# Kernel optimization log

Measured on AMD Instinct MI355X. Metric: run time of the kernel, lower is better.

## Reference

```python
import jax, jax.numpy as jnp
import numpy as np

B, L, C, N, TN = 1, 256, 128, 4, 4
CH = N * C  # 512, flattened hidden for routing projections
EPS = 1.1920929e-07  # torch.finfo(float32).eps (RMSNorm default eps)
LN_EPS = 1e-5
N_SINKHORN = 20  # training-mode iteration count


def sinkhorn_knopp(raw, n_iters):
    # raw: [..., n, n] real-valued logits -> doubly-stochastic matrix
    M = jnp.exp(raw)
    for _ in range(n_iters):
        M = M / jnp.sum(M, axis=-1, keepdims=True)  # row normalize
        M = M / jnp.sum(M, axis=-2, keepdims=True)  # col normalize
    return M


def setup_inputs() -> dict:
    key = jax.random.key(0)
    ks = jax.random.split(key, 8)
    s = 0.02
    eye = jnp.eye(N, dtype=jnp.float32)
    b_res = 2.0 * eye + (-2.0) * (1.0 - eye)
    return {
        "p": jax.random.normal(ks[0], (B, L, L, C), jnp.float32),
        "p_mask": jnp.ones((B, L, L), jnp.float32),
        "W_pre": jax.random.normal(ks[1], (N, CH), jnp.float32) * s,
        "W_post": jax.random.normal(ks[2], (N, CH), jnp.float32) * s,
        "W_res": jax.random.normal(ks[3], (N * N, CH), jnp.float32) * s,
        "b_pre": jnp.zeros((1, N), jnp.float32),
        "b_post": jnp.zeros((1, N), jnp.float32),
        "b_res": b_res,
        "alpha_pre": jnp.asarray(0.01, jnp.float32),
        "alpha_post": jnp.asarray(0.01, jnp.float32),
        "alpha_res": jnp.asarray(0.01, jnp.float32),
        "ln_g": jnp.ones((C,), jnp.float32),
        "ln_b": jnp.zeros((C,), jnp.float32),
        "W1": jax.random.normal(ks[4], (TN * C, C), jnp.float32) * s,
        "b1": jnp.zeros((TN * C,), jnp.float32),
        "W2": jax.random.normal(ks[5], (C, TN * C), jnp.float32) * s,
        "b2": jnp.zeros((C,), jnp.float32),
    }


def reference(p, p_mask, W_pre, W_post, W_res, b_pre, b_post, b_res,
              alpha_pre, alpha_post, alpha_res, ln_g, ln_b, W1, b1, W2, b2):
    # expand_input: [B,L,L,C] -> [B,L,L,n,C]
    x = jnp.broadcast_to(p[..., None, :], (B, L, L, N, C))
    # --- compute_mappings ---
    xf = x.reshape(B, L, L, CH)
    xn = xf * jax.lax.rsqrt(jnp.mean(xf * xf, axis=-1, keepdims=True) + EPS)
    H_pre_dyn = jnp.tanh(xn @ W_pre.T)                      # [B,L,L,n]
    H_post_dyn = jnp.tanh(xn @ W_post.T)                    # [B,L,L,n]
    H_res_dyn = jnp.tanh(xn @ W_res.T).reshape(B, L, L, N, N)
    H_pre = jax.nn.sigmoid(alpha_pre * H_pre_dyn + b_pre)   # [B,L,L,n]
    H_post = 2.0 * jax.nn.sigmoid(alpha_post * H_post_dyn + b_post)
    H_res = sinkhorn_knopp(alpha_res * H_res_dyn + b_res, N_SINKHORN)  # [B,L,L,n,n]
    # contract: H_pre [B,L,L,1,n] @ x [B,L,L,n,C] -> [B,L,L,C]
    p_c = jnp.einsum('blkn,blknc->blkc', H_pre, x)
    # --- PairTransition (LN -> Linear -> ReLU -> Linear, masked) ---
    mu = jnp.mean(p_c, axis=-1, keepdims=True)
    var = jnp.mean(jnp.square(p_c - mu), axis=-1, keepdims=True)
    m = (p_c - mu) * jax.lax.rsqrt(var + LN_EPS) * ln_g + ln_b
    h = jax.nn.relu(m @ W1.T + b1)                          # [B,L,L,TN*C]
    p_t = (h @ W2.T + b2) * p_mask[..., None]
    p_updated = p_c + p_t
    # expand back: H_post^T [B,L,L,n,1] * p_updated [B,L,L,1,C]
    p_expanded = H_post[..., :, None] * p_updated[..., None, :]
    # residual mixing: [B,L,L,n,n] @ [B,L,L,n,C]
    p_residual = jnp.einsum('blkmn,blknc->blkmc', H_res, x)
    return p_residual + p_expanded  # [B,L,L,n,C]
```

## Files before the change

### kernel.cpp

```cpp
#include <hip/hip_runtime.h>
#include <stdint.h>

#define LLTOT 65536
#define CDIM  128
#define TPIX  32

typedef float f32x4  __attribute__((ext_vector_type(4)));
typedef short s16x8  __attribute__((ext_vector_type(8)));

#define MFMA16(a, b, c) __builtin_amdgcn_mfma_f32_16x16x32_bf16((a), (b), (c), 0, 0, 0)

__device__ __align__(16) unsigned short g_wefff[2 * 4 * 64 * 8];
__device__ __align__(16) unsigned short g_w1gf[32 * 4 * 64 * 8];
__device__ __align__(16) unsigned short g_w2f16[16 * 8 * 64 * 8];
__device__ __align__(16) float  g_hA[512];
__device__ __align__(16) float  g_w1gs[512];

__device__ __forceinline__ unsigned short f2bf(float f) {
    union { float f; uint32_t u; } v; v.f = f;
    uint32_t u = v.u;
    return (unsigned short)((u + 0x7FFFu + ((u >> 16) & 1u)) >> 16);
}
__device__ __forceinline__ uint32_t pack2(float a, float b) {
    uint32_t r;
    asm("v_cvt_pk_bf16_f32 %0, %1, %2" : "=v"(r) : "v"(a), "v"(b));
    return r;
}
__device__ __forceinline__ float bf2f(uint32_t lo16) { return __uint_as_float(lo16 << 16); }

__device__ __forceinline__ float fast_tanh(float x) {
    float cx = fminf(fmaxf(x, -10.f), 10.f);
    float e = __expf(2.f * cx);
    return (e - 1.f) * __builtin_amdgcn_rcpf(e + 1.f);
}
__device__ __forceinline__ float fast_sig(float z) {
    return __builtin_amdgcn_rcpf(1.f + __expf(-z));
}

__global__ void prep_kernel(const float* __restrict__ Wpre, const float* __restrict__ Wpost,
                            const float* __restrict__ Wres, const float* __restrict__ W1,
                            const float* __restrict__ W2, const float* __restrict__ ln_g,
                            const float* __restrict__ ln_b, const float* __restrict__ b1) {
    int b = blockIdx.x, t = threadIdx.x;
    if (b == 264) {
        int j = t;
        float sg = 0.f, sb = 0.f;
        const float* row = W1 + j * 128;
        #pragma unroll 4
        for (int c = 0; c < 128; c += 4) {
            float4 wv = *(const float4*)(row + c);
            float4 gv = *(const float4*)(ln_g + c);
            float4 bv = *(const float4*)(ln_b + c);
            sg += wv.x*gv.x + wv.y*gv.y + wv.z*gv.z + wv.w*gv.w;
            sb += wv.x*bv.x + wv.y*bv.y + wv.z*bv.z + wv.w*bv.w;
        }
        g_hA[j]   = b1[j] + sb;
        g_w1gs[j] = sg;
        return;
    }
    int idx = b * 512 + t;
    if (idx < 4096) {
        int e = idx & 7, lane = (idx >> 3) & 63, kk = (idx >> 9) & 3, tile = idx >> 11;
        int o = tile * 16 + (lane & 15);
        int c = kk * 32 + (lane >> 4) * 8 + e;
        float v = 0.f;
        if (o < 4)        v = Wpre[o*512+c] + Wpre[o*512+128+c] + Wpre[o*512+256+c] + Wpre[o*512+384+c];
        else if (o < 8)   { int j = o - 4;  v = Wpost[j*512+c] + Wpost[j*512+128+c] + Wpost[j*512+256+c] + Wpost[j*512+384+c]; }
        else if (o < 24)  { int j = o - 8;  v = Wres[j*512+c] + Wres[j*512+128+c] + Wres[j*512+256+c] + Wres[j*512+384+c]; }
        g_wefff[idx] = f2bf(v);
    } else if (idx < 69632) {
        int d = idx - 4096;
        int e = d & 7, lane = (d >> 3) & 63, kk = (d >> 9) & 3, jt = d >> 11;
        int j = jt * 16 + (lane & 15);
        int c = kk * 32 + (lane >> 4) * 8 + e;
        g_w1gf[d] = f2bf(W1[j * 128 + c] * ln_g[c]);
    } else if (idx < 135168) {
        int d = idx - 69632;
        int e = d & 7, lane = (d >> 3) & 63, ct = (d >> 9) & 7, ksg = d >> 12;
        int c = ct * 16 + (lane & 15);
        int k = ksg * 32 + (lane >> 4) * 8 + e;
        g_w2f16[d] = f2bf(W2[c * 512 + k]);
    }
}

__global__ void __launch_bounds__(512, 2) fused_kernel(
    const float* __restrict__ p, const float* __restrict__ p_mask,
    const float* __restrict__ b_pre, const float* __restrict__ b_post, const float* __restrict__ b_res,
    const float* __restrict__ a_pre, const float* __restrict__ a_post, const float* __restrict__ a_res,
    const float* __restrict__ b2g, float* __restrict__ out)
{
    __shared__ __align__(16) unsigned short pf_lds[8 * 512];
    __shared__ __align__(16) unsigned short h16[32 * 512];
    __shared__ __align__(16) float A_s[128], B_s[128];
    __shared__ __align__(16) float2 simi_s[32];
    __shared__ __align__(16) float rms_s[32], mu_s[32], var_s[32];

    const int t = threadIdx.x;
    const int w = t >> 6, l = t & 63, lr = l & 15, lk = l >> 4;
    const size_t base = (size_t)blockIdx.x * TPIX;

    s16x8 aw01[8];
    #pragma unroll
    for (int kk = 0; kk < 2; ++kk)
        #pragma unroll
        for (int jt = 0; jt < 4; ++jt)
            aw01[kk * 4 + jt] = *(const s16x8*)(g_w1gf + ((size_t)((w * 4 + jt) * 4 + kk) * 64 + l) * 8);

    {
        int pix32 = t >> 4, ci = t & 15;
        const float* src = p + (base + pix32) * 128 + ci * 8;
        float4 va = *(const float4*)src;
        float4 vb = *(const float4*)(src + 4);
        float s  = va.x + va.y + va.z + va.w + vb.x + vb.y + vb.z + vb.w;
        float ss = va.x*va.x + va.y*va.y + va.z*va.z + va.w*va.w
                 + vb.x*vb.x + vb.y*vb.y + vb.z*vb.z + vb.w*vb.w;
        s += __shfl_xor(s, 1); ss += __shfl_xor(ss, 1);
        s += __shfl_xor(s, 2); ss += __shfl_xor(ss, 2);
        s += __shfl_xor(s, 4); ss += __shfl_xor(ss, 4);
        s += __shfl_xor(s, 8); ss += __shfl_xor(ss, 8);
        if (ci == 0) {
            float mu = s * (1.f / 128.f), mq = ss * (1.f / 128.f);
            rms_s[pix32] = rsqrtf(mq + 1.1920929e-07f);
            mu_s[pix32]  = mu;
            var_s[pix32] = mq - mu * mu;
        }
        uint4 u;
        u.x = pack2(va.x, va.y);
        u.y = pack2(va.z, va.w);
        u.z = pack2(vb.x, vb.y);
        u.w = pack2(vb.z, vb.w);
        uint32_t a16 = (uint32_t)((((pix32 >> 4) * 4 + (ci >> 2)) * 512
                     + ((pix32 & 15) + 16 * (ci & 3)) * 8));
        *(uint4*)(pf_lds + a16) = u;
    }
    __syncthreads();

    float M0 = 0.f, M1 = 0.f, M2 = 0.f, M3 = 0.f, sp = 0.f, hpm = 0.f;
    int mrow = 0, pix = 0;

    if (w < 2) {
        const int g = lk, pixl = lr;
        const size_t gpix = base + w * 16 + pixl;
        float apre = a_pre[0], apost = a_post[0], ares = a_res[0];
        float msk = p_mask[gpix];
        float bp0 = b_pre[0], bp1 = b_pre[1], bp2 = b_pre[2], bp3 = b_pre[3];
        float bq0 = b_post[0], bq1 = b_post[1], bq2 = b_post[2], bq3 = b_post[3];
        mrow = (g + 2) & 3;
        float br0 = b_res[mrow*4+0], br1 = b_res[mrow*4+1], br2 = b_res[mrow*4+2], br3 = b_res[mrow*4+3];

        float rv = rms_s[w * 16 + pixl];

        f32x4 y1 = {0.f, 0.f, 0.f, 0.f}, y2 = {0.f, 0.f, 0.f, 0.f};
        #pragma unroll
        for (int kk = 0; kk < 4; ++kk) {
            s16x8 bfr = *(const s16x8*)(pf_lds + (size_t)(w * 4 + kk) * 512 + l * 8);
            s16x8 a0 = *(const s16x8*)(g_wefff + ((size_t)(kk) * 64 + l) * 8);
            s16x8 a1 = *(const s16x8*)(g_wefff + ((size_t)(4 + kk) * 64 + l) * 8);
            y1 = MFMA16(a0, bfr, y1);
            y2 = MFMA16(a1, bfr, y2);
        }
        #pragma unroll
        for (int r = 0; r < 4; ++r) { y1[r] *= rv; y2[r] *= rv; }

        float sp_loc = fast_sig(apre * fast_tanh(y1[0]) + bp0)
                     + fast_sig(apre * fast_tanh(y1[1]) + bp1)
                     + fast_sig(apre * fast_tanh(y1[2]) + bp2)
                     + fast_sig(apre * fast_tanh(y1[3]) + bp3);
        sp = __shfl(sp_loc, pixl);

        float hp0 = 2.f * fast_sig(apost * fast_tanh(y1[0]) + bq0);
        float hp1 = 2.f * fast_sig(apost * fast_tanh(y1[1]) + bq1);
        float hp2 = 2.f * fast_sig(apost * fast_tanh(y1[2]) + bq2);
        float hp3 = 2.f * fast_sig(apost * fast_tanh(y1[3]) + bq3);

        bool lo = g < 2;
        M0 = __expf(ares * fast_tanh(lo ? y2[0] : y1[0]) + br0);
        M1 = __expf(ares * fast_tanh(lo ? y2[1] : y1[1]) + br1);
        M2 = __expf(ares * fast_tanh(lo ? y2[2] : y1[2]) + br2);
        M3 = __expf(ares * fast_tanh(lo ? y2[3] : y1[3]) + br3);

        float h0b = __shfl(hp0, pixl + 16);
        float h1b = __shfl(hp1, pixl + 16);
        float h2b = __shfl(hp2, pixl + 16);
        float h3b = __shfl(hp3, pixl + 16);
        hpm = (mrow & 2) ? ((mrow & 1) ? h3b : h2b) : ((mrow & 1) ? h1b : h0b);

        pix = w * 16 + pixl;
        B_s[pix * 4 + mrow] = hpm * msk;
        if (l < 16) {
            int px = w * 16 + lr;
            float istd = rsqrtf(sp * sp * var_s[px] + 1e-5f);
            simi_s[px] = make_float2(sp * istd, sp * mu_s[px] * istd);
        }
    }
    __syncthreads();

    if (w < 2) {
        #pragma unroll 1
        for (int it = 0; it < 20; ++it) {
            float ri = __builtin_amdgcn_rcpf(M0 + M1 + M2 + M3);
            M0 *= ri; M1 *= ri; M2 *= ri; M3 *= ri;
            float c0 = M0, c1 = M1, c2 = M2, c3 = M3;
            c0 += __shfl_xor(c0, 16); c1 += __shfl_xor(c1, 16); c2 += __shfl_xor(c2, 16); c3 += __shfl_xor(c3, 16);
            c0 += __shfl_xor(c0, 32); c1 += __shfl_xor(c1, 32); c2 += __shfl_xor(c2, 32); c3 += __shfl_xor(c3, 32);
            M0 *= __builtin_amdgcn_rcpf(c0); M1 *= __builtin_amdgcn_rcpf(c1);
            M2 *= __builtin_amdgcn_rcpf(c2); M3 *= __builtin_amdgcn_rcpf(c3);
        }
        float rm = M0 + M1 + M2 + M3;
        A_s[pix * 4 + mrow] = rm + hpm * sp;
    }

    s16x8 pfr[2][4];
    #pragma unroll
    for (int it = 0; it < 2; ++it)
        #pragma unroll
        for (int kk = 0; kk < 4; ++kk)
            pfr[it][kk] = *(const s16x8*)(pf_lds + (size_t)(it * 4 + kk) * 512 + l * 8);

    f32x4 acc1[4][2] = {};
    #pragma unroll
    for (int kk = 0; kk < 2; ++kk)
        #pragma unroll
        for (int jt = 0; jt < 4; ++jt) {
            s16x8 a = aw01[kk * 4 + jt];
            acc1[jt][0] = MFMA16(a, pfr[0][kk], acc1[jt][0]);
            acc1[jt][1] = MFMA16(a, pfr[1][kk], acc1[jt][1]);
        }
    #pragma unroll
    for (int kk = 2; kk < 4; ++kk)
        #pragma unroll
        for (int jt = 0; jt < 4; ++jt) {
            s16x8 a = *(const s16x8*)(g_w1gf + ((size_t)((w * 4 + jt) * 4 + kk) * 64 + l) * 8);
            acc1[jt][0] = MFMA16(a, pfr[0][kk], acc1[jt][0]);
            acc1[jt][1] = MFMA16(a, pfr[1][kk], acc1[jt][1]);
        }

    {
        float2 sim0 = simi_s[lr];
        float2 sim1 = simi_s[16 + lr];
        #pragma unroll
        for (int jt = 0; jt < 4; ++jt) {
            int j0 = w * 64 + jt * 16 + lk * 4;
            float4 wg = *(const float4*)(g_w1gs + j0);
            float4 ha = *(const float4*)(g_hA + j0);
            int ksg = w * 2 + (jt >> 1);
            int laneB = lr + 16 * ((jt & 1) * 2 + (lk >> 1));
            #pragma unroll
            for (int it = 0; it < 2; ++it) {
                float si = it ? sim1.x : sim0.x;
                float mi = it ? sim1.y : sim0.y;
                f32x4 v = acc1[jt][it];
                float h0 = fmaxf(fmaf(si, v[0], fmaf(-mi, wg.x, ha.x)), 0.f);
                float h1 = fmaxf(fmaf(si, v[1], fmaf(-mi, wg.y, ha.y)), 0.f);
                float h2 = fmaxf(fmaf(si, v[2], fmaf(-mi, wg.z, ha.z)), 0.f);
                float h3 = fmaxf(fmaf(si, v[3], fmaf(-mi, wg.w, ha.w)), 0.f);
                uint2 uu;
                uu.x = pack2(h0, h1);
                uu.y = pack2(h2, h3);
                *(uint2*)(h16 + (size_t)(ksg * 2 + it) * 512 + laneB * 8 + (lk & 1) * 4) = uu;
            }
        }
    }
    __syncthreads();

    f32x4 acc2[2] = {};
    #pragma unroll 4
    for (int ksg = 0; ksg < 16; ++ksg) {
        s16x8 a  = *(const s16x8*)(g_w2f16 + ((size_t)(ksg * 8 + w) * 64 + l) * 8);
        s16x8 b0 = *(const s16x8*)(h16 + (size_t)(ksg * 2 + 0) * 512 + l * 8);
        s16x8 b1 = *(const s16x8*)(h16 + (size_t)(ksg * 2 + 1) * 512 + l * 8);
        acc2[0] = MFMA16(a, b0, acc2[0]);
        acc2[1] = MFMA16(a, b1, acc2[1]);
    }

    const int c0 = w * 16 + lk * 4;
    float4 b2v = *(const float4*)(b2g + c0);
    #pragma unroll
    for (int it = 0; it < 2; ++it) {
        int i = it * 16 + lr;
        f32x4 Av = *(const f32x4*)(A_s + i * 4);
        f32x4 Bv = *(const f32x4*)(B_s + i * 4);
        const unsigned short* pe = pf_lds
            + ((size_t)(it * 4 + (w >> 1)) * 64 + ((w & 1) * 2 + (lk >> 1)) * 16 + lr) * 8
            + (lk & 1) * 4;
        uint2 pb = *(const uint2*)pe;
        float p0 = bf2f(pb.x & 0xffffu), p1 = __uint_as_float(pb.x & 0xffff0000u);
        float p2 = bf2f(pb.y & 0xffffu), p3 = __uint_as_float(pb.y & 0xffff0000u);
        float d0 = acc2[it][0] + b2v.x, d1 = acc2[it][1] + b2v.y;
        float d2 = acc2[it][2] + b2v.z, d3 = acc2[it][3] + b2v.w;
        float* og = out + (base + i) * 512 + c0;
        #pragma unroll
        for (int m = 0; m < 4; ++m) {
            f32x4 o;
            o[0] = Av[m] * p0 + Bv[m] * d0;
            o[1] = Av[m] * p1 + Bv[m] * d1;
            o[2] = Av[m] * p2 + Bv[m] * d2;
            o[3] = Av[m] * p3 + Bv[m] * d3;
            *(f32x4*)(og + m * 128) = o;
        }
    }
}

extern "C" void kernel_launch(void* const* d_in, const int* in_sizes, int n_in,
                              void* d_out, int out_size, void* d_ws, size_t ws_size,
                              hipStream_t stream) {
    const float* p      = (const float*)d_in[0];
    const float* p_mask = (const float*)d_in[1];
    const float* W_pre  = (const float*)d_in[2];
    const float* W_post = (const float*)d_in[3];
    const float* W_res  = (const float*)d_in[4];
    const float* b_pre  = (const float*)d_in[5];
    const float* b_post = (const float*)d_in[6];
    const float* b_res  = (const float*)d_in[7];
    const float* a_pre  = (const float*)d_in[8];
    const float* a_post = (const float*)d_in[9];
    const float* a_res  = (const float*)d_in[10];
    const float* ln_g   = (const float*)d_in[11];
    const float* ln_b   = (const float*)d_in[12];
    const float* W1     = (const float*)d_in[13];
    const float* b1     = (const float*)d_in[14];
    const float* W2     = (const float*)d_in[15];
    const float* b2     = (const float*)d_in[16];
    float* out = (float*)d_out;

    prep_kernel<<<265, 512, 0, stream>>>(W_pre, W_post, W_res, W1, W2, ln_g, ln_b, b1);
    fused_kernel<<<2048, 512, 0, stream>>>(p, p_mask, b_pre, b_post, b_res,
                                           a_pre, a_post, a_res, b2, out);
}
```

Measured before the change: 70.17 us.

## Process two 32-pixel tiles per block with persistent W1/W2 register fragments

Each block now loops over two 32-pixel tiles, halving the grid to 1024 blocks. The first W1 and W2 fragments are loaded into registers once and reused across both tiles. The plain __syncthreads calls become custom barriers that wait only on LDS counters, so outstanding global stores can drain during the next tile. The aim is to amortise per-block weight loads and launch cost, at the price of fewer blocks, less parallelism across CUs, and more register pressure.

```diff
diff --git a/kernel.cpp b/kernel.cpp
--- a/kernel.cpp
+++ b/kernel.cpp
@@ -3,12 +3,20 @@
 
 #define LLTOT 65536
 #define CDIM  128
-#define TPIX  32
+#define TILES 2
+#define NBLK  (LLTOT / (TILES * 32))
 
 typedef float f32x4  __attribute__((ext_vector_type(4)));
 typedef short s16x8  __attribute__((ext_vector_type(8)));
 
 #define MFMA16(a, b, c) __builtin_amdgcn_mfma_f32_16x16x32_bf16((a), (b), (c), 0, 0, 0)
+
+#define SYNCB() do {                                        \
+    __builtin_amdgcn_sched_barrier(0);                      \
+    asm volatile("s_waitcnt lgkmcnt(0)" ::: "memory");      \
+    __builtin_amdgcn_s_barrier();                           \
+    __builtin_amdgcn_sched_barrier(0);                      \
+} while (0)
 
 __device__ __align__(16) unsigned short g_wefff[2 * 4 * 64 * 8];
 __device__ __align__(16) unsigned short g_w1gf[32 * 4 * 64 * 8];
@@ -97,7 +105,7 @@
 
     const int t = threadIdx.x;
     const int w = t >> 6, l = t & 63, lr = l & 15, lk = l >> 4;
-    const size_t base = (size_t)blockIdx.x * TPIX;
+    const size_t blk_base = (size_t)blockIdx.x * (TILES * 32);
 
     s16x8 aw01[8];
     #pragma unroll
@@ -105,199 +113,216 @@
         #pragma unroll
         for (int jt = 0; jt < 4; ++jt)
             aw01[kk * 4 + jt] = *(const s16x8*)(g_w1gf + ((size_t)((w * 4 + jt) * 4 + kk) * 64 + l) * 8);
-
-    {
-        int pix32 = t >> 4, ci = t & 15;
-        const float* src = p + (base + pix32) * 128 + ci * 8;
-        float4 va = *(const float4*)src;
-        float4 vb = *(const float4*)(src + 4);
-        float s  = va.x + va.y + va.z + va.w + vb.x + vb.y + vb.z + vb.w;
-        float ss = va.x*va.x + va.y*va.y + va.z*va.z + va.w*va.w
-                 + vb.x*vb.x + vb.y*vb.y + vb.z*vb.z + vb.w*vb.w;
-        s += __shfl_xor(s, 1); ss += __shfl_xor(ss, 1);
-        s += __shfl_xor(s, 2); ss += __shfl_xor(ss, 2);
-        s += __shfl_xor(s, 4); ss += __shfl_xor(ss, 4);
-        s += __shfl_xor(s, 8); ss += __shfl_xor(ss, 8);
-        if (ci == 0) {
-            float mu = s * (1.f / 128.f), mq = ss * (1.f / 128.f);
-            rms_s[pix32] = rsqrtf(mq + 1.1920929e-07f);
-            mu_s[pix32]  = mu;
-            var_s[pix32] = mq - mu * mu;
-        }
-        uint4 u;
-        u.x = pack2(va.x, va.y);
-        u.y = pack2(va.z, va.w);
-        u.z = pack2(vb.x, vb.y);
-        u.w = pack2(vb.z, vb.w);
-        uint32_t a16 = (uint32_t)((((pix32 >> 4) * 4 + (ci >> 2)) * 512
-                     + ((pix32 & 15) + 16 * (ci & 3)) * 8));
-        *(uint4*)(pf_lds + a16) = u;
-    }
-    __syncthreads();
-
-    float M0 = 0.f, M1 = 0.f, M2 = 0.f, M3 = 0.f, sp = 0.f, hpm = 0.f;
-    int mrow = 0, pix = 0;
-
-    if (w < 2) {
-        const int g = lk, pixl = lr;
-        const size_t gpix = base + w * 16 + pixl;
-        float apre = a_pre[0], apost = a_post[0], ares = a_res[0];
-        float msk = p_mask[gpix];
-        float bp0 = b_pre[0], bp1 = b_pre[1], bp2 = b_pre[2], bp3 = b_pre[3];
-        float bq0 = b_post[0], bq1 = b_post[1], bq2 = b_post[2], bq3 = b_post[3];
-        mrow = (g + 2) & 3;
-        float br0 = b_res[mrow*4+0], br1 = b_res[mrow*4+1], br2 = b_res[mrow*4+2], br3 = b_res[mrow*4+3];
-
-        float rv = rms_s[w * 16 + pixl];
-
-        f32x4 y1 = {0.f, 0.f, 0.f, 0.f}, y2 = {0.f, 0.f, 0.f, 0.f};
-        #pragma unroll
-        for (int kk = 0; kk < 4; ++kk) {
-            s16x8 bfr = *(const s16x8*)(pf_lds + (size_t)(w * 4 + kk) * 512 + l * 8);
-            s16x8 a0 = *(const s16x8*)(g_wefff + ((size_t)(kk) * 64 + l) * 8);
-            s16x8 a1 = *(const s16x8*)(g_wefff + ((size_t)(4 + kk) * 64 + l) * 8);
-            y1 = MFMA16(a0, bfr, y1);
-            y2 = MFMA16(a1, bfr, y2);
-        }
-        #pragma unroll
-        for (int r = 0; r < 4; ++r) { y1[r] *= rv; y2[r] *= rv; }
-
-        float sp_loc = fast_sig(apre * fast_tanh(y1[0]) + bp0)
-                     + fast_sig(apre * fast_tanh(y1[1]) + bp1)
-                     + fast_sig(apre * fast_tanh(y1[2]) + bp2)
-                     + fast_sig(apre * fast_tanh(y1[3]) + bp3);
-        sp = __shfl(sp_loc, pixl);
-
-        float hp0 = 2.f * fast_sig(apost * fast_tanh(y1[0]) + bq0);
-        float hp1 = 2.f * fast_sig(apost * fast_tanh(y1[1]) + bq1);
-        float hp2 = 2.f * fast_sig(apost * fast_tanh(y1[2]) + bq2);
-        float hp3 = 2.f * fast_sig(apost * fast_tanh(y1[3]) + bq3);
-
-        bool lo = g < 2;
-        M0 = __expf(ares * fast_tanh(lo ? y2[0] : y1[0]) + br0);
-        M1 = __expf(ares * fast_tanh(lo ? y2[1] : y1[1]) + br1);
-        M2 = __expf(ares * fast_tanh(lo ? y2[2] : y1[2]) + br2);
-        M3 = __expf(ares * fast_tanh(lo ? y2[3] : y1[3]) + br3);
-
-        float h0b = __shfl(hp0, pixl + 16);
-        float h1b = __shfl(hp1, pixl + 16);
-        float h2b = __shfl(hp2, pixl + 16);
-        float h3b = __shfl(hp3, pixl + 16);
-        hpm = (mrow & 2) ? ((mrow & 1) ? h3b : h2b) : ((mrow & 1) ? h1b : h0b);
-
-        pix = w * 16 + pixl;
-        B_s[pix * 4 + mrow] = hpm * msk;
-        if (l < 16) {
-            int px = w * 16 + lr;
-            float istd = rsqrtf(sp * sp * var_s[px] + 1e-5f);
-            simi_s[px] = make_float2(sp * istd, sp * mu_s[px] * istd);
-        }
-    }
-    __syncthreads();
-
-    if (w < 2) {
-        #pragma unroll 1
-        for (int it = 0; it < 20; ++it) {
-            float ri = __builtin_amdgcn_rcpf(M0 + M1 + M2 + M3);
-            M0 *= ri; M1 *= ri; M2 *= ri; M3 *= ri;
-            float c0 = M0, c1 = M1, c2 = M2, c3 = M3;
-            c0 += __shfl_xor(c0, 16); c1 += __shfl_xor(c1, 16); c2 += __shfl_xor(c2, 16); c3 += __shfl_xor(c3, 16);
-            c0 += __shfl_xor(c0, 32); c1 += __shfl_xor(c1, 32); c2 += __shfl_xor(c2, 32); c3 += __shfl_xor(c3, 32);
-            M0 *= __builtin_amdgcn_rcpf(c0); M1 *= __builtin_amdgcn_rcpf(c1);
-            M2 *= __builtin_amdgcn_rcpf(c2); M3 *= __builtin_amdgcn_rcpf(c3);
-        }
-        float rm = M0 + M1 + M2 + M3;
-        A_s[pix * 4 + mrow] = rm + hpm * sp;
-    }
-
-    s16x8 pfr[2][4];
+    s16x8 w2p[2];
     #pragma unroll
-    for (int it = 0; it < 2; ++it)
-        #pragma unroll
-        for (int kk = 0; kk < 4; ++kk)
-            pfr[it][kk] = *(const s16x8*)(pf_lds + (size_t)(it * 4 + kk) * 512 + l * 8);
-
-    f32x4 acc1[4][2] = {};
-    #pragma unroll
-    for (int kk = 0; kk < 2; ++kk)
-        #pragma unroll
-        for (int jt = 0; jt < 4; ++jt) {
-            s16x8 a = aw01[kk * 4 + jt];
-            acc1[jt][0] = MFMA16(a, pfr[0][kk], acc1[jt][0]);
-            acc1[jt][1] = MFMA16(a, pfr[1][kk], acc1[jt][1]);
-        }
-    #pragma unroll
-    for (int kk = 2; kk < 4; ++kk)
-        #pragma unroll
-        for (int jt = 0; jt < 4; ++jt) {
-            s16x8 a = *(const s16x8*)(g_w1gf + ((size_t)((w * 4 + jt) * 4 + kk) * 64 + l) * 8);
-            acc1[jt][0] = MFMA16(a, pfr[0][kk], acc1[jt][0]);
-            acc1[jt][1] = MFMA16(a, pfr[1][kk], acc1[jt][1]);
-        }
-
-    {
-        float2 sim0 = simi_s[lr];
-        float2 sim1 = simi_s[16 + lr];
-        #pragma unroll
-        for (int jt = 0; jt < 4; ++jt) {
-            int j0 = w * 64 + jt * 16 + lk * 4;
-            float4 wg = *(const float4*)(g_w1gs + j0);
-            float4 ha = *(const float4*)(g_hA + j0);
-            int ksg = w * 2 + (jt >> 1);
-            int laneB = lr + 16 * ((jt & 1) * 2 + (lk >> 1));
-            #pragma unroll
-            for (int it = 0; it < 2; ++it) {
-                float si = it ? sim1.x : sim0.x;
-                float mi = it ? sim1.y : sim0.y;
-                f32x4 v = acc1[jt][it];
-                float h0 = fmaxf(fmaf(si, v[0], fmaf(-mi, wg.x, ha.x)), 0.f);
-                float h1 = fmaxf(fmaf(si, v[1], fmaf(-mi, wg.y, ha.y)), 0.f);
-                float h2 = fmaxf(fmaf(si, v[2], fmaf(-mi, wg.z, ha.z)), 0.f);
-                float h3 = fmaxf(fmaf(si, v[3], fmaf(-mi, wg.w, ha.w)), 0.f);
-                uint2 uu;
-                uu.x = pack2(h0, h1);
-                uu.y = pack2(h2, h3);
-                *(uint2*)(h16 + (size_t)(ksg * 2 + it) * 512 + laneB * 8 + (lk & 1) * 4) = uu;
-            }
-        }
-    }
-    __syncthreads();
-
-    f32x4 acc2[2] = {};
-    #pragma unroll 4
-    for (int ksg = 0; ksg < 16; ++ksg) {
-        s16x8 a  = *(const s16x8*)(g_w2f16 + ((size_t)(ksg * 8 + w) * 64 + l) * 8);
-        s16x8 b0 = *(const s16x8*)(h16 + (size_t)(ksg * 2 + 0) * 512 + l * 8);
-        s16x8 b1 = *(const s16x8*)(h16 + (size_t)(ksg * 2 + 1) * 512 + l * 8);
-        acc2[0] = MFMA16(a, b0, acc2[0]);
-        acc2[1] = MFMA16(a, b1, acc2[1]);
-    }
-
-    const int c0 = w * 16 + lk * 4;
-    float4 b2v = *(const float4*)(b2g + c0);
-    #pragma unroll
-    for (int it = 0; it < 2; ++it) {
-        int i = it * 16 + lr;
-        f32x4 Av = *(const f32x4*)(A_s + i * 4);
-        f32x4 Bv = *(const f32x4*)(B_s + i * 4);
-        const unsigned short* pe = pf_lds
-            + ((size_t)(it * 4 + (w >> 1)) * 64 + ((w & 1) * 2 + (lk >> 1)) * 16 + lr) * 8
-            + (lk & 1) * 4;
-        uint2 pb = *(const uint2*)pe;
-        float p0 = bf2f(pb.x & 0xffffu), p1 = __uint_as_float(pb.x & 0xffff0000u);
-        float p2 = bf2f(pb.y & 0xffffu), p3 = __uint_as_float(pb.y & 0xffff0000u);
-        float d0 = acc2[it][0] + b2v.x, d1 = acc2[it][1] + b2v.y;
-        float d2 = acc2[it][2] + b2v.z, d3 = acc2[it][3] + b2v.w;
-        float* og = out + (base + i) * 512 + c0;
-        #pragma unroll
-        for (int m = 0; m < 4; ++m) {
-            f32x4 o;
-            o[0] = Av[m] * p0 + Bv[m] * d0;
-            o[1] = Av[m] * p1 + Bv[m] * d1;
-            o[2] = Av[m] * p2 + Bv[m] * d2;
-            o[3] = Av[m] * p3 + Bv[m] * d3;
-            *(f32x4*)(og + m * 128) = o;
-        }
+    for (int ksg = 0; ksg < 2; ++ksg)
+        w2p[ksg] = *(const s16x8*)(g_w2f16 + ((size_t)(ksg * 8 + w) * 64 + l) * 8);
+
+    #pragma unroll 1
+    for (int tt = 0; tt < TILES; ++tt) {
+        const size_t base = blk_base + (size_t)tt * 32;
+
+        {
+            int pix32 = t >> 4, ci = t & 15;
+            const float* src = p + (base + pix32) * 128 + ci * 8;
+            float4 va = *(const float4*)src;
+            float4 vb = *(const float4*)(src + 4);
+            float s  = va.x + va.y + va.z + va.w + vb.x + vb.y + vb.z + vb.w;
+            float ss = va.x*va.x + va.y*va.y + va.z*va.z + va.w*va.w
+                     + vb.x*vb.x + vb.y*vb.y + vb.z*vb.z + vb.w*vb.w;
+            s += __shfl_xor(s, 1); ss += __shfl_xor(ss, 1);
+            s += __shfl_xor(s, 2); ss += __shfl_xor(ss, 2);
+            s += __shfl_xor(s, 4); ss += __shfl_xor(ss, 4);
+            s += __shfl_xor(s, 8); ss += __shfl_xor(ss, 8);
+            if (ci == 0) {
+                float mu = s * (1.f / 128.f), mq = ss * (1.f / 128.f);
+                rms_s[pix32] = rsqrtf(mq + 1.1920929e-07f);
+                mu_s[pix32]  = mu;
+                var_s[pix32] = mq - mu * mu;
+            }
+            uint4 u;
+            u.x = pack2(va.x, va.y);
+            u.y = pack2(va.z, va.w);
+            u.z = pack2(vb.x, vb.y);
+            u.w = pack2(vb.z, vb.w);
+            uint32_t a16 = (uint32_t)((((pix32 >> 4) * 4 + (ci >> 2)) * 512
+                         + ((pix32 & 15) + 16 * (ci & 3)) * 8));
+            *(uint4*)(pf_lds + a16) = u;
+        }
+        SYNCB();
+
+        float M0 = 0.f, M1 = 0.f, M2 = 0.f, M3 = 0.f, sp = 0.f, hpm = 0.f;
+        int mrow = 0, pix = 0;
+
+        if (w < 2) {
+            const int g = lk, pixl = lr;
+            const size_t gpix = base + w * 16 + pixl;
+            float apre = a_pre[0], apost = a_post[0], ares = a_res[0];
+            float msk = p_mask[gpix];
+            float bp0 = b_pre[0], bp1 = b_pre[1], bp2 = b_pre[2], bp3 = b_pre[3];
+            float bq0 = b_post[0], bq1 = b_post[1], bq2 = b_post[2], bq3 = b_post[3];
+            mrow = (g + 2) & 3;
+            float br0 = b_res[mrow*4+0], br1 = b_res[mrow*4+1], br2 = b_res[mrow*4+2], br3 = b_res[mrow*4+3];
+
+            float rv = rms_s[w * 16 + pixl];
+
+            f32x4 y1 = {0.f, 0.f, 0.f, 0.f}, y2 = {0.f, 0.f, 0.f, 0.f};
+            #pragma unroll
+            for (int kk = 0; kk < 4; ++kk) {
+                s16x8 bfr = *(const s16x8*)(pf_lds + (size_t)(w * 4 + kk) * 512 + l * 8);
+                s16x8 a0 = *(const s16x8*)(g_wefff + ((size_t)(kk) * 64 + l) * 8);
+                s16x8 a1 = *(const s16x8*)(g_wefff + ((size_t)(4 + kk) * 64 + l) * 8);
+                y1 = MFMA16(a0, bfr, y1);
+                y2 = MFMA16(a1, bfr, y2);
+            }
+            #pragma unroll
+            for (int r = 0; r < 4; ++r) { y1[r] *= rv; y2[r] *= rv; }
+
+            float sp_loc = fast_sig(apre * fast_tanh(y1[0]) + bp0)
+                         + fast_sig(apre * fast_tanh(y1[1]) + bp1)
+                         + fast_sig(apre * fast_tanh(y1[2]) + bp2)
+                         + fast_sig(apre * fast_tanh(y1[3]) + bp3);
+            sp = __shfl(sp_loc, pixl);
+
+            float hp0 = 2.f * fast_sig(apost * fast_tanh(y1[0]) + bq0);
+            float hp1 = 2.f * fast_sig(apost * fast_tanh(y1[1]) + bq1);
+            float hp2 = 2.f * fast_sig(apost * fast_tanh(y1[2]) + bq2);
+            float hp3 = 2.f * fast_sig(apost * fast_tanh(y1[3]) + bq3);
+
+            bool lo = g < 2;
+            M0 = __expf(ares * fast_tanh(lo ? y2[0] : y1[0]) + br0);
+            M1 = __expf(ares * fast_tanh(lo ? y2[1] : y1[1]) + br1);
+            M2 = __expf(ares * fast_tanh(lo ? y2[2] : y1[2]) + br2);
+            M3 = __expf(ares * fast_tanh(lo ? y2[3] : y1[3]) + br3);
+
+            float h0b = __shfl(hp0, pixl + 16);
+            float h1b = __shfl(hp1, pixl + 16);
+            float h2b = __shfl(hp2, pixl + 16);
+            float h3b = __shfl(hp3, pixl + 16);
+            hpm = (mrow & 2) ? ((mrow & 1) ? h3b : h2b) : ((mrow & 1) ? h1b : h0b);
+
+            pix = w * 16 + pixl;
+            B_s[pix * 4 + mrow] = hpm * msk;
+            if (l < 16) {
+                int px = w * 16 + lr;
+                float istd = rsqrtf(sp * sp * var_s[px] + 1e-5f);
+                simi_s[px] = make_float2(sp * istd, sp * mu_s[px] * istd);
+            }
+        }
+        SYNCB();
+
+        if (w < 2) {
+            #pragma unroll 1
+            for (int it = 0; it < 20; ++it) {
+                float ri = __builtin_amdgcn_rcpf(M0 + M1 + M2 + M3);
+                M0 *= ri; M1 *= ri; M2 *= ri; M3 *= ri;
+                float c0 = M0, c1 = M1, c2 = M2, c3 = M3;
+                c0 += __shfl_xor(c0, 16); c1 += __shfl_xor(c1, 16); c2 += __shfl_xor(c2, 16); c3 += __shfl_xor(c3, 16);
+                c0 += __shfl_xor(c0, 32); c1 += __shfl_xor(c1, 32); c2 += __shfl_xor(c2, 32); c3 += __shfl_xor(c3, 32);
+                M0 *= __builtin_amdgcn_rcpf(c0); M1 *= __builtin_amdgcn_rcpf(c1);
+                M2 *= __builtin_amdgcn_rcpf(c2); M3 *= __builtin_amdgcn_rcpf(c3);
+            }
+            float rm = M0 + M1 + M2 + M3;
+            A_s[pix * 4 + mrow] = rm + hpm * sp;
+        }
+
+        s16x8 pfr[2][4];
+        #pragma unroll
+        for (int it = 0; it < 2; ++it)
+            #pragma unroll
+            for (int kk = 0; kk < 4; ++kk)
+                pfr[it][kk] = *(const s16x8*)(pf_lds + (size_t)(it * 4 + kk) * 512 + l * 8);
+
+        f32x4 acc1[4][2] = {};
+        #pragma unroll
+        for (int kk = 0; kk < 2; ++kk)
+            #pragma unroll
+            for (int jt = 0; jt < 4; ++jt) {
+                s16x8 a = aw01[kk * 4 + jt];
+                acc1[jt][0] = MFMA16(a, pfr[0][kk], acc1[jt][0]);
+                acc1[jt][1] = MFMA16(a, pfr[1][kk], acc1[jt][1]);
+            }
+        #pragma unroll
+        for (int kk = 2; kk < 4; ++kk)
+            #pragma unroll
+            for (int jt = 0; jt < 4; ++jt) {
+                s16x8 a = *(const s16x8*)(g_w1gf + ((size_t)((w * 4 + jt) * 4 + kk) * 64 + l) * 8);
+                acc1[jt][0] = MFMA16(a, pfr[0][kk], acc1[jt][0]);
+                acc1[jt][1] = MFMA16(a, pfr[1][kk], acc1[jt][1]);
+            }
+
+        {
+            float2 sim0 = simi_s[lr];
+            float2 sim1 = simi_s[16 + lr];
+            #pragma unroll
+            for (int jt = 0; jt < 4; ++jt) {
+                int j0 = w * 64 + jt * 16 + lk * 4;
+                float4 wg = *(const float4*)(g_w1gs + j0);
+                float4 ha = *(const float4*)(g_hA + j0);
+                int ksg = w * 2 + (jt >> 1);
+                int laneB = lr + 16 * ((jt & 1) * 2 + (lk >> 1));
+                #pragma unroll
+                for (int it = 0; it < 2; ++it) {
+                    float si = it ? sim1.x : sim0.x;
+                    float mi = it ? sim1.y : sim0.y;
+                    f32x4 v = acc1[jt][it];
+                    float h0 = fmaxf(fmaf(si, v[0], fmaf(-mi, wg.x, ha.x)), 0.f);
+                    float h1 = fmaxf(fmaf(si, v[1], fmaf(-mi, wg.y, ha.y)), 0.f);
+                    float h2 = fmaxf(fmaf(si, v[2], fmaf(-mi, wg.z, ha.z)), 0.f);
+                    float h3 = fmaxf(fmaf(si, v[3], fmaf(-mi, wg.w, ha.w)), 0.f);
+                    uint2 uu;
+                    uu.x = pack2(h0, h1);
+                    uu.y = pack2(h2, h3);
+                    *(uint2*)(h16 + (size_t)(ksg * 2 + it) * 512 + laneB * 8 + (lk & 1) * 4) = uu;
+                }
+            }
+        }
+        SYNCB();
+
+        f32x4 acc2[2] = {};
+        #pragma unroll
+        for (int ksg = 0; ksg < 2; ++ksg) {
+            s16x8 b0 = *(const s16x8*)(h16 + (size_t)(ksg * 2 + 0) * 512 + l * 8);
+            s16x8 b1 = *(const s16x8*)(h16 + (size_t)(ksg * 2 + 1) * 512 + l * 8);
+            acc2[0] = MFMA16(w2p[ksg], b0, acc2[0]);
+            acc2[1] = MFMA16(w2p[ksg], b1, acc2[1]);
+        }
+        #pragma unroll 4
+        for (int ksg = 2; ksg < 16; ++ksg) {
+            s16x8 a  = *(const s16x8*)(g_w2f16 + ((size_t)(ksg * 8 + w) * 64 + l) * 8);
+            s16x8 b0 = *(const s16x8*)(h16 + (size_t)(ksg * 2 + 0) * 512 + l * 8);
+            s16x8 b1 = *(const s16x8*)(h16 + (size_t)(ksg * 2 + 1) * 512 + l * 8);
+            acc2[0] = MFMA16(a, b0, acc2[0]);
+            acc2[1] = MFMA16(a, b1, acc2[1]);
+        }
+
+        const int c0 = w * 16 + lk * 4;
+        float4 b2v = *(const float4*)(b2g + c0);
+        #pragma unroll
+        for (int it = 0; it < 2; ++it) {
+            int i = it * 16 + lr;
+            f32x4 Av = *(const f32x4*)(A_s + i * 4);
+            f32x4 Bv = *(const f32x4*)(B_s + i * 4);
+            const unsigned short* pe = pf_lds
+                + ((size_t)(it * 4 + (w >> 1)) * 64 + ((w & 1) * 2 + (lk >> 1)) * 16 + lr) * 8
+                + (lk & 1) * 4;
+            uint2 pb = *(const uint2*)pe;
+            float p0 = bf2f(pb.x & 0xffffu), p1 = __uint_as_float(pb.x & 0xffff0000u);
+            float p2 = bf2f(pb.y & 0xffffu), p3 = __uint_as_float(pb.y & 0xffff0000u);
+            float d0 = acc2[it][0] + b2v.x, d1 = acc2[it][1] + b2v.y;
+            float d2 = acc2[it][2] + b2v.z, d3 = acc2[it][3] + b2v.w;
+            float* og = out + (base + i) * 512 + c0;
+            #pragma unroll
+            for (int m = 0; m < 4; ++m) {
+                f32x4 o;
+                o[0] = Av[m] * p0 + Bv[m] * d0;
+                o[1] = Av[m] * p1 + Bv[m] * d1;
+                o[2] = Av[m] * p2 + Bv[m] * d2;
+                o[3] = Av[m] * p3 + Bv[m] * d3;
+                *(f32x4*)(og + m * 128) = o;
+            }
+        }
+        SYNCB();
     }
 }
 
@@ -324,6 +349,6 @@
     float* out = (float*)d_out;
 
     prep_kernel<<<265, 512, 0, stream>>>(W_pre, W_post, W_res, W1, W2, ln_g, ln_b, b1);
-    fused_kernel<<<2048, 512, 0, stream>>>(p, p_mask, b_pre, b_post, b_res,
+    fused_kernel<<<NBLK, 512, 0, stream>>>(p, p_mask, b_pre, b_post, b_res,
                                            a_pre, a_post, a_res, b2, out);
 }
```

Result: slower. 94.64 us (+34.9%).
